# Kernel optimization log

Measured on AMD Instinct MI355X. Metric: run time of the kernel, lower is better.

Reference implementation:

```python
import jax, jax.numpy as jnp
import numpy as np

BETA = 1.0  # lagr_softmax default inverse temperature

def setup_inputs() -> dict:
    key = jax.random.key(0)
    ks = jax.random.split(key, 5)
    B, Tq, Tk, Eq, Ek, E, H = 2, 2048, 2048, 1024, 1024, 1024, 16
    s = lambda d: 1.0 / np.sqrt(d)
    return {
        "gq": jax.random.normal(ks[0], (B, Tq, Eq), jnp.float32),
        "gk": jax.random.normal(ks[1], (B, Tk, Ek), jnp.float32),
        "WQ": jax.random.normal(ks[2], (E, Eq), jnp.float32) * s(Eq),
        "WK": jax.random.normal(ks[3], (E, Ek), jnp.float32) * s(Ek),
        "Wmix": jax.random.normal(ks[4], (1, H), jnp.float32) * s(H),
    }

def reference(gq, gk, WQ, WK, Wmix):
    B, Tq, _ = gq.shape
    H = Wmix.shape[1]
    E = WQ.shape[0]
    D = E // H
    # Linear projections (bias=False): x @ W.T
    q = (gq @ WQ.T).reshape(B, Tq, H, D)          # (B,Tq,H,D)
    k = (gk @ WK.T).reshape(B, -1, H, D)          # (B,Tk,H,D)
    # scores q @ k^T per head: (B,H,Tq,Tk)
    a = jnp.einsum('bqhd,bkhd->bhqk', q, k)
    # mix_heads: Linear(n_heads -> 1) applied over head axis
    a = jnp.einsum('bhqk,h->bqk', a, Wmix[0])     # (B,Tq,Tk)
    # lagr_softmax: (1/beta) * logsumexp(beta * a, dim=-1)
    out = jax.nn.logsumexp(BETA * a, axis=-1) / BETA  # (B,Tq)
    return out[:, None, :]                        # (B,1,Tq) matching torch shape
```

## Files before the change

kernel.cpp:

```cpp
#include <hip/hip_runtime.h>
#include <hip/hip_bf16.h>
#include <math.h>

#define B_    2
#define TQ    2048
#define TK    2048
#define E_    1024
#define MTOT  4096

typedef __attribute__((ext_vector_type(8))) short bf16x8;
typedef __attribute__((ext_vector_type(4))) float f32x4;

__device__ __forceinline__ unsigned short f2bf(float x) {
  unsigned int u = __float_as_uint(x);
  u += 0x7fff + ((u >> 16) & 1);
  return (unsigned short)(u >> 16);
}

__device__ __forceinline__ void load_lds16(const void* g, void* l) {
  __builtin_amdgcn_global_load_lds(
      (const __attribute__((address_space(1))) unsigned int*)g,
      (__attribute__((address_space(3))) unsigned int*)l, 16, 0, 0);
}

__global__ void prep_kernel(const float* __restrict__ gq, const float* __restrict__ gk,
                            const float* __restrict__ WQ, const float* __restrict__ WK,
                            const float* __restrict__ Wmix,
                            unsigned short* __restrict__ gqb, unsigned short* __restrict__ gkb,
                            unsigned short* __restrict__ wqb, unsigned short* __restrict__ wkb) {
  const int NGQ = (B_ * TQ * E_) / 4;
  const int NW  = (E_ * E_) / 4;
  const int total = 2 * NGQ + 2 * NW;
  for (int idx = blockIdx.x * blockDim.x + threadIdx.x; idx < total;
       idx += gridDim.x * blockDim.x) {
    const float4* src; unsigned short* dst; int local; float scale = 1.0f;
    if (idx < NGQ)            { src = (const float4*)gq; dst = gqb; local = idx; }
    else if (idx < 2 * NGQ)   { src = (const float4*)gk; dst = gkb; local = idx - NGQ; }
    else if (idx < 2*NGQ+NW)  { src = (const float4*)WQ; dst = wqb; local = idx - 2*NGQ;
                                scale = Wmix[local >> 14]; }
    else                      { src = (const float4*)WK; dst = wkb; local = idx - 2*NGQ - NW; }
    float4 v = src[local];
    ushort4 o;
    o.x = f2bf(v.x * scale); o.y = f2bf(v.y * scale);
    o.z = f2bf(v.z * scale); o.w = f2bf(v.w * scale);
    ((ushort4*)dst)[local] = o;
  }
}

__global__ __launch_bounds__(256) void proj_kernel(
    const unsigned short* __restrict__ gqb, const unsigned short* __restrict__ gkb,
    const unsigned short* __restrict__ wqb, const unsigned short* __restrict__ wkb,
    unsigned short* __restrict__ qp, unsigned short* __restrict__ kp) {
  const unsigned short* A = blockIdx.z ? gkb : gqb;
  const unsigned short* W = blockIdx.z ? wkb : wqb;
  unsigned short* C       = blockIdx.z ? kp  : qp;
  const int K = E_, N = E_;
  __shared__ unsigned short As[128 * 32];
  __shared__ unsigned short Bs[128 * 32];
  const int tid = threadIdx.x, wave = tid >> 6, lane = tid & 63;
  const int wrow = wave >> 1, wcol = wave & 1;
  const int m0 = blockIdx.y * 128, n0 = blockIdx.x * 128;
  f32x4 acc[4][4] = {};
  const int sr = wave * 32 + (lane >> 2);
  const int sc = (lane & 3) * 8;
  for (int k0 = 0; k0 < K; k0 += 32) {
    __syncthreads();
    load_lds16(A + (size_t)(m0 + sr) * K + k0 + sc,      As + (wave * 32) * 32);
    load_lds16(A + (size_t)(m0 + sr + 16) * K + k0 + sc, As + (wave * 32 + 16) * 32);
    load_lds16(W + (size_t)(n0 + sr) * K + k0 + sc,      Bs + (wave * 32) * 32);
    load_lds16(W + (size_t)(n0 + sr + 16) * K + k0 + sc, Bs + (wave * 32 + 16) * 32);
    __syncthreads();
    bf16x8 af[4], bw[4];
#pragma unroll
    for (int f = 0; f < 4; ++f) {
      af[f] = *(const bf16x8*)(As + (wrow * 64 + f * 16 + (lane & 15)) * 32 + (lane >> 4) * 8);
      bw[f] = *(const bf16x8*)(Bs + (wcol * 64 + f * 16 + (lane & 15)) * 32 + (lane >> 4) * 8);
    }
#pragma unroll
    for (int fi = 0; fi < 4; ++fi)
#pragma unroll
      for (int fj = 0; fj < 4; ++fj)
        acc[fi][fj] = __builtin_amdgcn_mfma_f32_16x16x32_bf16(af[fi], bw[fj], acc[fi][fj], 0, 0, 0);
  }
#pragma unroll
  for (int fi = 0; fi < 4; ++fi)
#pragma unroll
    for (int fj = 0; fj < 4; ++fj)
#pragma unroll
      for (int j = 0; j < 4; ++j) {
        int row = m0 + wrow * 64 + fi * 16 + (lane >> 4) * 4 + j;
        int col = n0 + wcol * 64 + fj * 16 + (lane & 15);
        C[(size_t)row * N + col] = f2bf(acc[fi][fj][j]);
      }
}

__global__ __launch_bounds__(256) void score_lse_kernel(
    const unsigned short* __restrict__ qp, const unsigned short* __restrict__ kp,
    float2* __restrict__ partials) {
  const int b = blockIdx.z;
  const unsigned short* A  = qp + (size_t)b * TQ * E_;
  const unsigned short* Bm = kp + (size_t)b * TK * E_;
  const int K = E_;
  __shared__ unsigned short As[128 * 32];
  __shared__ unsigned short Bs[128 * 32];
  __shared__ float redM[2][128];
  __shared__ float redS[2][128];
  const int tid = threadIdx.x, wave = tid >> 6, lane = tid & 63;
  const int wrow = wave >> 1, wcol = wave & 1;
  const int m0 = blockIdx.y * 128, n0 = blockIdx.x * 128;
  f32x4 acc[4][4] = {};
  const int sr = wave * 32 + (lane >> 2);
  const int sc = (lane & 3) * 8;
  for (int k0 = 0; k0 < K; k0 += 32) {
    __syncthreads();
    load_lds16(A  + (size_t)(m0 + sr) * K + k0 + sc,      As + (wave * 32) * 32);
    load_lds16(A  + (size_t)(m0 + sr + 16) * K + k0 + sc, As + (wave * 32 + 16) * 32);
    load_lds16(Bm + (size_t)(n0 + sr) * K + k0 + sc,      Bs + (wave * 32) * 32);
    load_lds16(Bm + (size_t)(n0 + sr + 16) * K + k0 + sc, Bs + (wave * 32 + 16) * 32);
    __syncthreads();
    bf16x8 af[4], bk[4];
#pragma unroll
    for (int f = 0; f < 4; ++f) {
      af[f] = *(const bf16x8*)(As + (wrow * 64 + f * 16 + (lane & 15)) * 32 + (lane >> 4) * 8);
      bk[f] = *(const bf16x8*)(Bs + (wcol * 64 + f * 16 + (lane & 15)) * 32 + (lane >> 4) * 8);
    }
#pragma unroll
    for (int fi = 0; fi < 4; ++fi)
#pragma unroll
      for (int fj = 0; fj < 4; ++fj)
        acc[fi][fj] = __builtin_amdgcn_mfma_f32_16x16x32_bf16(af[fi], bk[fj], acc[fi][fj], 0, 0, 0);
  }
  const int grp = lane >> 4, li = lane & 15;
#pragma unroll
  for (int fi = 0; fi < 4; ++fi) {
#pragma unroll
    for (int j = 0; j < 4; ++j) {
      float m = fmaxf(fmaxf(acc[fi][0][j], acc[fi][1][j]),
                      fmaxf(acc[fi][2][j], acc[fi][3][j]));
#pragma unroll
      for (int msk = 1; msk < 16; msk <<= 1) m = fmaxf(m, __shfl_xor(m, msk, 64));
      float s = 0.f;
#pragma unroll
      for (int fj = 0; fj < 4; ++fj) s += expf(acc[fi][fj][j] - m);
#pragma unroll
      for (int msk = 1; msk < 16; msk <<= 1) s += __shfl_xor(s, msk, 64);
      if (li == 0) {
        int row = wrow * 64 + fi * 16 + grp * 4 + j;
        redM[wcol][row] = m;
        redS[wcol][row] = s;
      }
    }
  }
  __syncthreads();
  if (tid < 128) {
    float mA = redM[0][tid], mB = redM[1][tid];
    float M = fmaxf(mA, mB);
    float S = redS[0][tid] * expf(mA - M) + redS[1][tid] * expf(mB - M);
    int qrow = b * TQ + m0 + tid;
    partials[(size_t)qrow * 16 + blockIdx.x] = make_float2(M, S);
  }
}

__global__ void finalize_kernel(const float2* __restrict__ partials, float* __restrict__ out) {
  int r = blockIdx.x * blockDim.x + threadIdx.x;
  if (r >= MTOT) return;
  const float2* p = partials + (size_t)r * 16;
  float M = p[0].x;
#pragma unroll
  for (int i = 1; i < 16; ++i) M = fmaxf(M, p[i].x);
  float S = 0.f;
#pragma unroll
  for (int i = 0; i < 16; ++i) S += p[i].y * expf(p[i].x - M);
  out[r] = logf(S) + M;
}

extern "C" void kernel_launch(void* const* d_in, const int* in_sizes, int n_in,
                              void* d_out, int out_size, void* d_ws, size_t ws_size,
                              hipStream_t stream) {
  const float* gq   = (const float*)d_in[0];
  const float* gk   = (const float*)d_in[1];
  const float* WQ   = (const float*)d_in[2];
  const float* WK   = (const float*)d_in[3];
  const float* Wmix = (const float*)d_in[4];
  float* out = (float*)d_out;

  char* ws = (char*)d_ws;
  unsigned short* gqb = (unsigned short*)(ws);
  unsigned short* gkb = (unsigned short*)(ws + 8388608);
  unsigned short* wqb = (unsigned short*)(ws + 16777216);
  unsigned short* wkb = (unsigned short*)(ws + 18874368);
  unsigned short* qp  = (unsigned short*)(ws + 20971520);
  unsigned short* kp  = (unsigned short*)(ws + 29360128);
  float2* partials    = (float2*)(ws + 37748736);

  hipLaunchKernelGGL(prep_kernel, dim3(1024), dim3(256), 0, stream,
                     gq, gk, WQ, WK, Wmix, gqb, gkb, wqb, wkb);
  hipLaunchKernelGGL(proj_kernel, dim3(8, 32, 2), dim3(256), 0, stream,
                     gqb, gkb, wqb, wkb, qp, kp);
  hipLaunchKernelGGL(score_lse_kernel, dim3(16, 16, 2), dim3(256), 0, stream,
                     qp, kp, partials);
  hipLaunchKernelGGL(finalize_kernel, dim3(16), dim3(256), 0, stream,
                     partials, out);
}
```

Baseline: 152.0 us.

## Double-buffer LDS tiles in projection and score GEMMs to overlap loads

Both GEMM kernels now use two LDS buffers per operand. The next K-slice is issued with global_load_lds while MFMAs run on the current slice, and only one barrier per iteration remains instead of two. The aim is to hide global-to-LDS latency behind compute. LDS usage per block doubles to 32KB for the tiles, which can reduce occupancy. Correctness depends on the end-of-iteration barrier also waiting for the async LDS loads (vmcnt) to finish.

```diff
diff --git a/kernel.cpp b/kernel.cpp
--- a/kernel.cpp
+++ b/kernel.cpp
@@ -55,32 +55,45 @@
   const unsigned short* W = blockIdx.z ? wkb : wqb;
   unsigned short* C       = blockIdx.z ? kp  : qp;
   const int K = E_, N = E_;
-  __shared__ unsigned short As[128 * 32];
-  __shared__ unsigned short Bs[128 * 32];
+  __shared__ unsigned short As[2][128 * 32];
+  __shared__ unsigned short Bs[2][128 * 32];
   const int tid = threadIdx.x, wave = tid >> 6, lane = tid & 63;
   const int wrow = wave >> 1, wcol = wave & 1;
   const int m0 = blockIdx.y * 128, n0 = blockIdx.x * 128;
   f32x4 acc[4][4] = {};
   const int sr = wave * 32 + (lane >> 2);
   const int sc = (lane & 3) * 8;
-  for (int k0 = 0; k0 < K; k0 += 32) {
-    __syncthreads();
-    load_lds16(A + (size_t)(m0 + sr) * K + k0 + sc,      As + (wave * 32) * 32);
-    load_lds16(A + (size_t)(m0 + sr + 16) * K + k0 + sc, As + (wave * 32 + 16) * 32);
-    load_lds16(W + (size_t)(n0 + sr) * K + k0 + sc,      Bs + (wave * 32) * 32);
-    load_lds16(W + (size_t)(n0 + sr + 16) * K + k0 + sc, Bs + (wave * 32 + 16) * 32);
-    __syncthreads();
+  const unsigned short* gA0 = A + (size_t)(m0 + sr) * K + sc;
+  const unsigned short* gA1 = A + (size_t)(m0 + sr + 16) * K + sc;
+  const unsigned short* gB0 = W + (size_t)(n0 + sr) * K + sc;
+  const unsigned short* gB1 = W + (size_t)(n0 + sr + 16) * K + sc;
+
+#define STAGE_P(b, k0)                                         \
+  do {                                                         \
+    load_lds16(gA0 + (k0), &As[b][(wave * 32) * 32]);          \
+    load_lds16(gA1 + (k0), &As[b][(wave * 32 + 16) * 32]);     \
+    load_lds16(gB0 + (k0), &Bs[b][(wave * 32) * 32]);          \
+    load_lds16(gB1 + (k0), &Bs[b][(wave * 32 + 16) * 32]);     \
+  } while (0)
+
+  STAGE_P(0, 0);
+  __syncthreads();
+  const int NT = K / 32;
+  for (int t = 0; t < NT; ++t) {
+    const int cur = t & 1;
     bf16x8 af[4], bw[4];
 #pragma unroll
     for (int f = 0; f < 4; ++f) {
-      af[f] = *(const bf16x8*)(As + (wrow * 64 + f * 16 + (lane & 15)) * 32 + (lane >> 4) * 8);
-      bw[f] = *(const bf16x8*)(Bs + (wcol * 64 + f * 16 + (lane & 15)) * 32 + (lane >> 4) * 8);
+      af[f] = *(const bf16x8*)(&As[cur][(wrow * 64 + f * 16 + (lane & 15)) * 32 + (lane >> 4) * 8]);
+      bw[f] = *(const bf16x8*)(&Bs[cur][(wcol * 64 + f * 16 + (lane & 15)) * 32 + (lane >> 4) * 8]);
     }
+    if (t + 1 < NT) STAGE_P(cur ^ 1, (t + 1) * 32);
 #pragma unroll
     for (int fi = 0; fi < 4; ++fi)
 #pragma unroll
       for (int fj = 0; fj < 4; ++fj)
         acc[fi][fj] = __builtin_amdgcn_mfma_f32_16x16x32_bf16(af[fi], bw[fj], acc[fi][fj], 0, 0, 0);
+    __syncthreads();
   }
 #pragma unroll
   for (int fi = 0; fi < 4; ++fi)
@@ -92,6 +105,7 @@
         int col = n0 + wcol * 64 + fj * 16 + (lane & 15);
         C[(size_t)row * N + col] = f2bf(acc[fi][fj][j]);
       }
+#undef STAGE_P
 }
 
 __global__ __launch_bounds__(256) void score_lse_kernel(
@@ -101,8 +115,8 @@
   const unsigned short* A  = qp + (size_t)b * TQ * E_;
   const unsigned short* Bm = kp + (size_t)b * TK * E_;
   const int K = E_;
-  __shared__ unsigned short As[128 * 32];
-  __shared__ unsigned short Bs[128 * 32];
+  __shared__ unsigned short As[2][128 * 32];
+  __shared__ unsigned short Bs[2][128 * 32];
   __shared__ float redM[2][128];
   __shared__ float redS[2][128];
   const int tid = threadIdx.x, wave = tid >> 6, lane = tid & 63;
@@ -111,25 +125,39 @@
   f32x4 acc[4][4] = {};
   const int sr = wave * 32 + (lane >> 2);
   const int sc = (lane & 3) * 8;
-  for (int k0 = 0; k0 < K; k0 += 32) {
-    __syncthreads();
-    load_lds16(A  + (size_t)(m0 + sr) * K + k0 + sc,      As + (wave * 32) * 32);
-    load_lds16(A  + (size_t)(m0 + sr + 16) * K + k0 + sc, As + (wave * 32 + 16) * 32);
-    load_lds16(Bm + (size_t)(n0 + sr) * K + k0 + sc,      Bs + (wave * 32) * 32);
-    load_lds16(Bm + (size_t)(n0 + sr + 16) * K + k0 + sc, Bs + (wave * 32 + 16) * 32);
-    __syncthreads();
+  const unsigned short* gA0 = A  + (size_t)(m0 + sr) * K + sc;
+  const unsigned short* gA1 = A  + (size_t)(m0 + sr + 16) * K + sc;
+  const unsigned short* gB0 = Bm + (size_t)(n0 + sr) * K + sc;
+  const unsigned short* gB1 = Bm + (size_t)(n0 + sr + 16) * K + sc;
+
+#define STAGE_S(bf, k0)                                        \
+  do {                                                         \
+    load_lds16(gA0 + (k0), &As[bf][(wave * 32) * 32]);         \
+    load_lds16(gA1 + (k0), &As[bf][(wave * 32 + 16) * 32]);    \
+    load_lds16(gB0 + (k0), &Bs[bf][(wave * 32) * 32]);         \
+    load_lds16(gB1 + (k0), &Bs[bf][(wave * 32 + 16) * 32]);    \
+  } while (0)
+
+  STAGE_S(0, 0);
+  __syncthreads();
+  const int NT = K / 32;
+  for (int t = 0; t < NT; ++t) {
+    const int cur = t & 1;
     bf16x8 af[4], bk[4];
 #pragma unroll
     for (int f = 0; f < 4; ++f) {
-      af[f] = *(const bf16x8*)(As + (wrow * 64 + f * 16 + (lane & 15)) * 32 + (lane >> 4) * 8);
-      bk[f] = *(const bf16x8*)(Bs + (wcol * 64 + f * 16 + (lane & 15)) * 32 + (lane >> 4) * 8);
+      af[f] = *(const bf16x8*)(&As[cur][(wrow * 64 + f * 16 + (lane & 15)) * 32 + (lane >> 4) * 8]);
+      bk[f] = *(const bf16x8*)(&Bs[cur][(wcol * 64 + f * 16 + (lane & 15)) * 32 + (lane >> 4) * 8]);
     }
+    if (t + 1 < NT) STAGE_S(cur ^ 1, (t + 1) * 32);
 #pragma unroll
     for (int fi = 0; fi < 4; ++fi)
 #pragma unroll
       for (int fj = 0; fj < 4; ++fj)
         acc[fi][fj] = __builtin_amdgcn_mfma_f32_16x16x32_bf16(af[fi], bk[fj], acc[fi][fj], 0, 0, 0);
-  }
+    __syncthreads();
+  }
+#undef STAGE_S
   const int grp = lane >> 4, li = lane & 15;
 #pragma unroll
   for (int fi = 0; fi < 4; ++fi) {
```

Result: no change. 150.7 us (-0.8%).

## Use 256x256 tiles with double-buffered async LDS pipeline in both GEMMs

Applied to the files above, without the earlier changes.

Both the projection and score GEMMs move from 128x128 tiles with 4 waves and single-buffered K=32 steps to 256x256 tiles with 8 waves and K=64 double-buffered LDS staging. Global-to-LDS loads for the next K slice are interleaved with MFMA quadrants, using manual vmcnt/lgkmcnt waits, barriers and s_setprio. The goal is to hide load latency and raise arithmetic intensity per block. In exchange the grids shrink (128 blocks per GEMM), so CU utilization may drop, and register pressure rises with 128 accumulator values per lane.

```diff
diff --git a/kernel.cpp b/kernel.cpp
--- a/kernel.cpp
+++ b/kernel.cpp
@@ -22,6 +22,78 @@
       (const __attribute__((address_space(1))) unsigned int*)g,
       (__attribute__((address_space(3))) unsigned int*)l, 16, 0, 0);
 }
+
+#define BARRIER() do { asm volatile("" ::: "memory"); __builtin_amdgcn_s_barrier(); asm volatile("" ::: "memory"); } while (0)
+#define WAIT_VM4()   asm volatile("s_waitcnt vmcnt(4)" ::: "memory")
+#define WAIT_VM0()   asm volatile("s_waitcnt vmcnt(0)" ::: "memory")
+#define WAIT_LGKM0() asm volatile("s_waitcnt lgkmcnt(0)" ::: "memory")
+
+__device__ __forceinline__ void stage_half(const unsigned short* gsrc, unsigned short* lds,
+                                           int tid, int half, int kt) {
+  const unsigned short* g = gsrc + (size_t)(half * 128 + (tid >> 3)) * E_ + (size_t)kt * 64 + (tid & 7) * 8;
+  unsigned short* l = lds + half * 8192 + tid * 8;
+  load_lds16(g, l);
+  load_lds16(g + 64 * E_, l + 4096);
+}
+
+#define READ_A(mh)                                                            \
+  do {                                                                        \
+    _Pragma("unroll") for (int f = 0; f < 4; ++f)                             \
+      _Pragma("unroll") for (int ks = 0; ks < 2; ++ks)                        \
+        a[f][ks] = *(const bf16x8*)(Ac + ((wm * 128 + (mh) * 64 + f * 16 + li16) * 64 + ks * 32 + hi4 * 8)); \
+  } while (0)
+
+#define READ_B(nh)                                                            \
+  do {                                                                        \
+    _Pragma("unroll") for (int g = 0; g < 2; ++g)                             \
+      _Pragma("unroll") for (int ks = 0; ks < 2; ++ks)                        \
+        b[nh][g][ks] = *(const bf16x8*)(Bc + ((wn * 64 + (nh) * 32 + g * 16 + li16) * 64 + ks * 32 + hi4 * 8)); \
+  } while (0)
+
+#define MFMA_Q(mh, nh)                                                        \
+  do {                                                                        \
+    __builtin_amdgcn_s_setprio(1);                                            \
+    _Pragma("unroll") for (int ks = 0; ks < 2; ++ks)                          \
+      _Pragma("unroll") for (int f = 0; f < 4; ++f)                           \
+        _Pragma("unroll") for (int g = 0; g < 2; ++g)                         \
+          acc[(mh) * 4 + f][(nh) * 2 + g] = __builtin_amdgcn_mfma_f32_16x16x32_bf16( \
+              a[f][ks], b[nh][g][ks], acc[(mh) * 4 + f][(nh) * 2 + g], 0, 0, 0); \
+    __builtin_amdgcn_s_setprio(0);                                            \
+  } while (0)
+
+#define GEMM_PIPELINE()                                                       \
+  do {                                                                        \
+    stage_half(Ag, As[0], tid, 0, 0);                                         \
+    stage_half(Ag, As[0], tid, 1, 0);                                         \
+    stage_half(Bg, Bs[0], tid, 0, 0);                                         \
+    stage_half(Bg, Bs[0], tid, 1, 0);                                         \
+    stage_half(Bg, Bs[1], tid, 0, 1);                                         \
+    stage_half(Bg, Bs[1], tid, 1, 1);                                         \
+    WAIT_VM4();                                                               \
+    BARRIER();                                                                \
+    for (int t = 0; t < 16; ++t) {                                            \
+      const int c = t & 1;                                                    \
+      const int nx = (t + 1) & 15;                                            \
+      const int nx2 = (t + 2) & 15;                                           \
+      unsigned short* Ac = As[c];                                             \
+      unsigned short* Bc = Bs[c];                                             \
+                                                                     \
+      READ_A(0); READ_B(0);                                                   \
+      stage_half(Ag, As[c ^ 1], tid, 0, nx);                                  \
+      BARRIER(); WAIT_LGKM0(); MFMA_Q(0, 0); BARRIER();                       \
+                                                                     \
+      READ_B(1);                                                              \
+      stage_half(Ag, As[c ^ 1], tid, 1, nx);                                  \
+      BARRIER(); WAIT_LGKM0(); MFMA_Q(0, 1); BARRIER();                       \
+                                                                     \
+      READ_A(1);                                                              \
+      stage_half(Bg, Bs[c], tid, 0, nx2);                                     \
+      BARRIER(); WAIT_LGKM0(); MFMA_Q(1, 0); BARRIER();                       \
+                                                                     \
+      stage_half(Bg, Bs[c], tid, 1, nx2);                                     \
+      WAIT_VM4(); BARRIER(); MFMA_Q(1, 1); BARRIER();                         \
+    }                                                                         \
+  } while (0)
 
 __global__ void prep_kernel(const float* __restrict__ gq, const float* __restrict__ gk,
                             const float* __restrict__ WQ, const float* __restrict__ WK,
@@ -47,130 +119,92 @@
   }
 }
 
-__global__ __launch_bounds__(256) void proj_kernel(
+__global__ __launch_bounds__(512, 2) void proj_kernel(
     const unsigned short* __restrict__ gqb, const unsigned short* __restrict__ gkb,
     const unsigned short* __restrict__ wqb, const unsigned short* __restrict__ wkb,
     unsigned short* __restrict__ qp, unsigned short* __restrict__ kp) {
-  const unsigned short* A = blockIdx.z ? gkb : gqb;
-  const unsigned short* W = blockIdx.z ? wkb : wqb;
-  unsigned short* C       = blockIdx.z ? kp  : qp;
-  const int K = E_, N = E_;
-  __shared__ unsigned short As[128 * 32];
-  __shared__ unsigned short Bs[128 * 32];
+  __shared__ __align__(16) unsigned short As[2][16384];
+  __shared__ __align__(16) unsigned short Bs[2][16384];
+  const int m0 = blockIdx.y * 256, n0 = blockIdx.x * 256;
+  const unsigned short* Ag = (blockIdx.z ? gkb : gqb) + (size_t)m0 * E_;
+  const unsigned short* Bg = (blockIdx.z ? wkb : wqb) + (size_t)n0 * E_;
+  unsigned short* C        = (blockIdx.z ? kp  : qp);
   const int tid = threadIdx.x, wave = tid >> 6, lane = tid & 63;
-  const int wrow = wave >> 1, wcol = wave & 1;
-  const int m0 = blockIdx.y * 128, n0 = blockIdx.x * 128;
-  f32x4 acc[4][4] = {};
-  const int sr = wave * 32 + (lane >> 2);
-  const int sc = (lane & 3) * 8;
-  for (int k0 = 0; k0 < K; k0 += 32) {
-    __syncthreads();
-    load_lds16(A + (size_t)(m0 + sr) * K + k0 + sc,      As + (wave * 32) * 32);
-    load_lds16(A + (size_t)(m0 + sr + 16) * K + k0 + sc, As + (wave * 32 + 16) * 32);
-    load_lds16(W + (size_t)(n0 + sr) * K + k0 + sc,      Bs + (wave * 32) * 32);
-    load_lds16(W + (size_t)(n0 + sr + 16) * K + k0 + sc, Bs + (wave * 32 + 16) * 32);
-    __syncthreads();
-    bf16x8 af[4], bw[4];
-#pragma unroll
-    for (int f = 0; f < 4; ++f) {
-      af[f] = *(const bf16x8*)(As + (wrow * 64 + f * 16 + (lane & 15)) * 32 + (lane >> 4) * 8);
-      bw[f] = *(const bf16x8*)(Bs + (wcol * 64 + f * 16 + (lane & 15)) * 32 + (lane >> 4) * 8);
-    }
-#pragma unroll
-    for (int fi = 0; fi < 4; ++fi)
-#pragma unroll
-      for (int fj = 0; fj < 4; ++fj)
-        acc[fi][fj] = __builtin_amdgcn_mfma_f32_16x16x32_bf16(af[fi], bw[fj], acc[fi][fj], 0, 0, 0);
-  }
-#pragma unroll
-  for (int fi = 0; fi < 4; ++fi)
-#pragma unroll
-    for (int fj = 0; fj < 4; ++fj)
+  const int wm = wave >> 2, wn = wave & 3, li16 = lane & 15, hi4 = lane >> 4;
+  f32x4 acc[8][4] = {};
+  bf16x8 a[4][2];
+  bf16x8 b[2][2][2];
+  GEMM_PIPELINE();
+#pragma unroll
+  for (int mr = 0; mr < 8; ++mr)
+#pragma unroll
+    for (int nr = 0; nr < 4; ++nr)
 #pragma unroll
       for (int j = 0; j < 4; ++j) {
-        int row = m0 + wrow * 64 + fi * 16 + (lane >> 4) * 4 + j;
-        int col = n0 + wcol * 64 + fj * 16 + (lane & 15);
-        C[(size_t)row * N + col] = f2bf(acc[fi][fj][j]);
+        int row = m0 + wm * 128 + mr * 16 + hi4 * 4 + j;
+        int col = n0 + wn * 64 + nr * 16 + li16;
+        C[(size_t)row * E_ + col] = f2bf(acc[mr][nr][j]);
       }
-}
-
-__global__ __launch_bounds__(256) void score_lse_kernel(
+  WAIT_VM0();
+}
+
+__global__ __launch_bounds__(512, 2) void score_lse_kernel(
     const unsigned short* __restrict__ qp, const unsigned short* __restrict__ kp,
     float2* __restrict__ partials) {
-  const int b = blockIdx.z;
-  const unsigned short* A  = qp + (size_t)b * TQ * E_;
-  const unsigned short* Bm = kp + (size_t)b * TK * E_;
-  const int K = E_;
-  __shared__ unsigned short As[128 * 32];
-  __shared__ unsigned short Bs[128 * 32];
-  __shared__ float redM[2][128];
-  __shared__ float redS[2][128];
+  __shared__ __align__(16) unsigned short As[2][16384];
+  __shared__ __align__(16) unsigned short Bs[2][16384];
+  __shared__ float redM[4][256];
+  __shared__ float redS[4][256];
+  const int bb = blockIdx.z;
+  const int m0 = blockIdx.y * 256, n0 = blockIdx.x * 256;
+  const unsigned short* Ag = qp + (size_t)bb * TQ * E_ + (size_t)m0 * E_;
+  const unsigned short* Bg = kp + (size_t)bb * TK * E_ + (size_t)n0 * E_;
   const int tid = threadIdx.x, wave = tid >> 6, lane = tid & 63;
-  const int wrow = wave >> 1, wcol = wave & 1;
-  const int m0 = blockIdx.y * 128, n0 = blockIdx.x * 128;
-  f32x4 acc[4][4] = {};
-  const int sr = wave * 32 + (lane >> 2);
-  const int sc = (lane & 3) * 8;
-  for (int k0 = 0; k0 < K; k0 += 32) {
-    __syncthreads();
-    load_lds16(A  + (size_t)(m0 + sr) * K + k0 + sc,      As + (wave * 32) * 32);
-    load_lds16(A  + (size_t)(m0 + sr + 16) * K + k0 + sc, As + (wave * 32 + 16) * 32);
-    load_lds16(Bm + (size_t)(n0 + sr) * K + k0 + sc,      Bs + (wave * 32) * 32);
-    load_lds16(Bm + (size_t)(n0 + sr + 16) * K + k0 + sc, Bs + (wave * 32 + 16) * 32);
-    __syncthreads();
-    bf16x8 af[4], bk[4];
-#pragma unroll
-    for (int f = 0; f < 4; ++f) {
-      af[f] = *(const bf16x8*)(As + (wrow * 64 + f * 16 + (lane & 15)) * 32 + (lane >> 4) * 8);
-      bk[f] = *(const bf16x8*)(Bs + (wcol * 64 + f * 16 + (lane & 15)) * 32 + (lane >> 4) * 8);
-    }
-#pragma unroll
-    for (int fi = 0; fi < 4; ++fi)
-#pragma unroll
-      for (int fj = 0; fj < 4; ++fj)
-        acc[fi][fj] = __builtin_amdgcn_mfma_f32_16x16x32_bf16(af[fi], bk[fj], acc[fi][fj], 0, 0, 0);
-  }
-  const int grp = lane >> 4, li = lane & 15;
-#pragma unroll
-  for (int fi = 0; fi < 4; ++fi) {
+  const int wm = wave >> 2, wn = wave & 3, li16 = lane & 15, hi4 = lane >> 4;
+  f32x4 acc[8][4] = {};
+  bf16x8 a[4][2];
+  bf16x8 b[2][2][2];
+  GEMM_PIPELINE();
+#pragma unroll
+  for (int mr = 0; mr < 8; ++mr) {
 #pragma unroll
     for (int j = 0; j < 4; ++j) {
-      float m = fmaxf(fmaxf(acc[fi][0][j], acc[fi][1][j]),
-                      fmaxf(acc[fi][2][j], acc[fi][3][j]));
+      float m = fmaxf(fmaxf(acc[mr][0][j], acc[mr][1][j]),
+                      fmaxf(acc[mr][2][j], acc[mr][3][j]));
 #pragma unroll
       for (int msk = 1; msk < 16; msk <<= 1) m = fmaxf(m, __shfl_xor(m, msk, 64));
       float s = 0.f;
 #pragma unroll
-      for (int fj = 0; fj < 4; ++fj) s += expf(acc[fi][fj][j] - m);
+      for (int nr = 0; nr < 4; ++nr) s += expf(acc[mr][nr][j] - m);
 #pragma unroll
       for (int msk = 1; msk < 16; msk <<= 1) s += __shfl_xor(s, msk, 64);
-      if (li == 0) {
-        int row = wrow * 64 + fi * 16 + grp * 4 + j;
-        redM[wcol][row] = m;
-        redS[wcol][row] = s;
+      if (li16 == 0) {
+        int row = wm * 128 + mr * 16 + hi4 * 4 + j;
+        redM[wn][row] = m;
+        redS[wn][row] = s;
       }
     }
   }
   __syncthreads();
-  if (tid < 128) {
-    float mA = redM[0][tid], mB = redM[1][tid];
-    float M = fmaxf(mA, mB);
-    float S = redS[0][tid] * expf(mA - M) + redS[1][tid] * expf(mB - M);
-    int qrow = b * TQ + m0 + tid;
-    partials[(size_t)qrow * 16 + blockIdx.x] = make_float2(M, S);
+  if (tid < 256) {
+    float M = fmaxf(fmaxf(redM[0][tid], redM[1][tid]), fmaxf(redM[2][tid], redM[3][tid]));
+    float S = redS[0][tid] * expf(redM[0][tid] - M) + redS[1][tid] * expf(redM[1][tid] - M) +
+              redS[2][tid] * expf(redM[2][tid] - M) + redS[3][tid] * expf(redM[3][tid] - M);
+    int qrow = bb * TQ + m0 + tid;
+    partials[(size_t)qrow * 8 + blockIdx.x] = make_float2(M, S);
   }
 }
 
 __global__ void finalize_kernel(const float2* __restrict__ partials, float* __restrict__ out) {
   int r = blockIdx.x * blockDim.x + threadIdx.x;
   if (r >= MTOT) return;
-  const float2* p = partials + (size_t)r * 16;
+  const float2* p = partials + (size_t)r * 8;
   float M = p[0].x;
 #pragma unroll
-  for (int i = 1; i < 16; ++i) M = fmaxf(M, p[i].x);
+  for (int i = 1; i < 8; ++i) M = fmaxf(M, p[i].x);
   float S = 0.f;
 #pragma unroll
-  for (int i = 0; i < 16; ++i) S += p[i].y * expf(p[i].x - M);
+  for (int i = 0; i < 8; ++i) S += p[i].y * expf(p[i].x - M);
   out[r] = logf(S) + M;
 }
 
@@ -195,9 +229,9 @@
 
   hipLaunchKernelGGL(prep_kernel, dim3(1024), dim3(256), 0, stream,
                      gq, gk, WQ, WK, Wmix, gqb, gkb, wqb, wkb);
-  hipLaunchKernelGGL(proj_kernel, dim3(8, 32, 2), dim3(256), 0, stream,
+  hipLaunchKernelGGL(proj_kernel, dim3(4, 16, 2), dim3(512), 0, stream,
                      gqb, gkb, wqb, wkb, qp, kp);
-  hipLaunchKernelGGL(score_lse_kernel, dim3(16, 16, 2), dim3(256), 0, stream,
+  hipLaunchKernelGGL(score_lse_kernel, dim3(8, 8, 2), dim3(512), 0, stream,
                      qp, kp, partials);
   hipLaunchKernelGGL(finalize_kernel, dim3(16), dim3(256), 0, stream,
                      partials, out);
```

New measurement: 189.4 us. +24.6%, slower.
